# Kernel tuning notes

Hardware: AMD Instinct MI355X
Metric: run time of the kernel (lower is better)

Reference implementation:

```python
import jax, jax.numpy as jnp
import numpy as np

NUM_HEADS = 16
KEY_DEPTH = 1024


def setup_inputs() -> dict:
    key = jax.random.key(0)
    ks = jax.random.split(key, 7)
    B, L, D = 2, 2048, 1024
    scale = 1.0 / np.sqrt(D)
    return {
        "query_antecedent": jax.random.normal(ks[0], (B, L, D), jnp.float32),
        "memory_antecedent": jax.random.normal(ks[1], (B, L, D), jnp.float32),
        "bias": jax.random.normal(ks[2], (1, 1, L, L), jnp.float32),
        "Wq": jax.random.normal(ks[3], (D, KEY_DEPTH), jnp.float32) * scale,
        "Wk": jax.random.normal(ks[4], (D, KEY_DEPTH), jnp.float32) * scale,
        "Wv": jax.random.normal(ks[5], (D, KEY_DEPTH), jnp.float32) * scale,
        "Wo": jax.random.normal(ks[6], (KEY_DEPTH, D), jnp.float32) * scale,
    }


def _split_heads(x, h):
    # [B, L, D] -> [B, H, L, D/H]
    b, l, d = x.shape
    return x.reshape(b, l, h, d // h).transpose(0, 2, 1, 3)


def reference(query_antecedent, memory_antecedent, bias, Wq, Wk, Wv, Wo):
    h = NUM_HEADS
    d_head = KEY_DEPTH // h
    q = _split_heads(query_antecedent @ Wq, h) * (d_head ** -0.5)
    k = _split_heads(memory_antecedent @ Wk, h)
    v = _split_heads(memory_antecedent @ Wv, h)
    # [B, H, Lq, Lk]
    logits = jnp.einsum("bhqd,bhkd->bhqk", q, k) + bias
    weights = jax.nn.softmax(logits, axis=-1)
    x = jnp.einsum("bhqk,bhkd->bhqd", weights, v)
    # combine heads: [B, H, L, d] -> [B, L, H*d]
    b, _, l, d = x.shape
    x = x.transpose(0, 2, 1, 3).reshape(b, l, h * d)
    return x @ Wo
```

## Files before the change

### kernel.cpp

```cpp
#include <hip/hip_runtime.h>
#include <hip/hip_bf16.h>


typedef __attribute__((ext_vector_type(8))) short short8;
typedef __attribute__((ext_vector_type(4))) short short4v;
typedef __attribute__((ext_vector_type(4))) float float4v;

#define BATCH 2
#define LSEQ 2048
#define DMODEL 1024
#define NHEADS 16
#define DHEAD 64
#define MROWS 4096
#define QKVLD 3072

__global__ __launch_bounds__(256)
void convert_kernel(const float* __restrict__ qa, const float* __restrict__ ma,
                    __hip_bfloat16* __restrict__ qo, __hip_bfloat16* __restrict__ mo)
{
    const size_t i = ((size_t)blockIdx.x * 256 + threadIdx.x) * 8;
    const float* src = blockIdx.y ? ma : qa;
    __hip_bfloat16* dst = blockIdx.y ? mo : qo;
    float4 v0 = *reinterpret_cast<const float4*>(src + i);
    float4 v1 = *reinterpret_cast<const float4*>(src + i + 4);
    union { __hip_bfloat16 h[8]; int4 v; } pk;
    pk.h[0] = (__hip_bfloat16)v0.x; pk.h[1] = (__hip_bfloat16)v0.y;
    pk.h[2] = (__hip_bfloat16)v0.z; pk.h[3] = (__hip_bfloat16)v0.w;
    pk.h[4] = (__hip_bfloat16)v1.x; pk.h[5] = (__hip_bfloat16)v1.y;
    pk.h[6] = (__hip_bfloat16)v1.z; pk.h[7] = (__hip_bfloat16)v1.w;
    *reinterpret_cast<int4*>(dst + i) = pk.v;
}

__global__ __launch_bounds__(256)
void transpose_w_kernel(const float* __restrict__ W0, const float* __restrict__ W1,
                        const float* __restrict__ W2, const float* __restrict__ W3,
                        __hip_bfloat16* __restrict__ T0, __hip_bfloat16* __restrict__ T1,
                        __hip_bfloat16* __restrict__ T2, __hip_bfloat16* __restrict__ T3)
{
    __shared__ __hip_bfloat16 T[64][68];

    const float* W; __hip_bfloat16* D;
    if      (blockIdx.z == 0) { W = W0; D = T0; }
    else if (blockIdx.z == 1) { W = W1; D = T1; }
    else if (blockIdx.z == 2) { W = W2; D = T2; }
    else                      { W = W3; D = T3; }

    const int t  = threadIdx.x;
    const int n0 = blockIdx.x * 64;
    const int k0 = blockIdx.y * 64;

#pragma unroll
    for (int p = 0; p < 4; ++p) {
        const int r = p * 16 + (t >> 4);
        const int c = (t & 15) * 4;
        float4 v = *reinterpret_cast<const float4*>(&W[(size_t)(k0 + r) * DMODEL + n0 + c]);
        union { __hip_bfloat16 h[4]; ushort4 v; } pk;
        pk.h[0] = (__hip_bfloat16)v.x; pk.h[1] = (__hip_bfloat16)v.y;
        pk.h[2] = (__hip_bfloat16)v.z; pk.h[3] = (__hip_bfloat16)v.w;
        *reinterpret_cast<ushort4*>(&T[r][c]) = pk.v;
    }
    __syncthreads();
#pragma unroll
    for (int p = 0; p < 2; ++p) {
        const int n  = p * 32 + (t & 31);
        const int kc = (t >> 5) * 8;
        union { __hip_bfloat16 h[8]; int4 v; } pk;
#pragma unroll
        for (int j = 0; j < 8; ++j) pk.h[j] = T[kc + j][n];
        *reinterpret_cast<int4*>(&D[(size_t)(n0 + n) * DMODEL + k0 + kc]) = pk.v;
    }
}

#define GBK 64

__global__ __launch_bounds__(256, 2)
void gemm_bt_kernel(const __hip_bfloat16* __restrict__ A0,
                    const __hip_bfloat16* __restrict__ A1, int nsplit,
                    float alpha0, float alpha1,
                    const __hip_bfloat16* __restrict__ Bt,
                    float* __restrict__ Cf, __hip_bfloat16* __restrict__ Cb,
                    int K, int ldc, int nbx)
{
    __shared__ __hip_bfloat16 As[128][GBK];
    __shared__ __hip_bfloat16 Bs[128][GBK];

    const int t    = threadIdx.x;
    const int w    = t >> 6;
    const int lane = t & 63;
    const int l15  = lane & 15;
    const int lq   = lane >> 4;
    const int wm   = (w >> 1) * 64;
    const int wn   = (w & 1) * 64;

    const int nwg  = gridDim.x;
    const int c    = blockIdx.x & 7;
    const int q    = blockIdx.x >> 3;
    const int mper = (nwg >> 3) / nbx;
    const int m0   = (c * mper + q / nbx) * 128;
    const int n0   = (q % nbx) * 128;

    const __hip_bfloat16* A = (n0 < nsplit) ? A0 : A1;
    const float alpha = (n0 < nsplit) ? alpha0 : alpha1;

    const int lrow = lane >> 3;
    const int lch  = (lane & 7) ^ lrow;

    float4v acc[4][4];
#pragma unroll
    for (int mi = 0; mi < 4; ++mi)
#pragma unroll
        for (int ni = 0; ni < 4; ++ni) acc[mi][ni] = (float4v){0.f, 0.f, 0.f, 0.f};

    for (int k0 = 0; k0 < K; k0 += GBK) {
        __syncthreads();
#pragma unroll
        for (int i = 0; i < 4; ++i) {
            const int rb = (w * 4 + i) * 8;
            const int r  = rb + lrow;
            __builtin_amdgcn_global_load_lds(
                (const __attribute__((address_space(1))) void*)
                    (A + (size_t)(m0 + r) * K + k0 + lch * 8),
                (__attribute__((address_space(3))) void*)&As[rb][0], 16, 0, 0);
            __builtin_amdgcn_global_load_lds(
                (const __attribute__((address_space(1))) void*)
                    (Bt + (size_t)(n0 + r) * K + k0 + lch * 8),
                (__attribute__((address_space(3))) void*)&Bs[rb][0], 16, 0, 0);
        }
        asm volatile("s_waitcnt vmcnt(0)" ::: "memory");
        __syncthreads();

#pragma unroll
        for (int kh = 0; kh < 2; ++kh) {
            short8 af[4], bf[4];
#pragma unroll
            for (int mi = 0; mi < 4; ++mi) {
                const int r = wm + mi * 16 + l15;
                af[mi] = *reinterpret_cast<const short8*>(
                    &As[r][(((kh << 2) | lq) ^ (r & 7)) << 3]);
            }
#pragma unroll
            for (int ni = 0; ni < 4; ++ni) {
                const int r = wn + ni * 16 + l15;
                bf[ni] = *reinterpret_cast<const short8*>(
                    &Bs[r][(((kh << 2) | lq) ^ (r & 7)) << 3]);
            }
#pragma unroll
            for (int mi = 0; mi < 4; ++mi)
#pragma unroll
                for (int ni = 0; ni < 4; ++ni)
                    acc[mi][ni] = __builtin_amdgcn_mfma_f32_16x16x32_bf16(
                        af[mi], bf[ni], acc[mi][ni], 0, 0, 0);
        }
    }

#pragma unroll
    for (int mi = 0; mi < 4; ++mi)
#pragma unroll
        for (int ni = 0; ni < 4; ++ni)
#pragma unroll
            for (int r = 0; r < 4; ++r) {
                const int row = m0 + wm + mi * 16 + lq * 4 + r;
                const int col = n0 + wn + ni * 16 + l15;
                const float v = acc[mi][ni][r] * alpha;
                if (Cf) Cf[(size_t)row * ldc + col] = v;
                else    Cb[(size_t)row * ldc + col] = (__hip_bfloat16)v;
            }
}

#define KSTR 68
#define PSTR 132

__global__ __launch_bounds__(512, 4)
void attn_mfma_kernel(const __hip_bfloat16* __restrict__ QKV,
                      const float* __restrict__ bias,
                      __hip_bfloat16* __restrict__ X)
{
    __shared__ __hip_bfloat16 Ks[128][KSTR];
    __shared__ __hip_bfloat16 Vt[64][PSTR];

    const int t   = threadIdx.x;
    const int w   = t >> 6;
    const int l15 = t & 15;
    const int lq  = (t & 63) >> 4;

    const int bid = blockIdx.x;
    const int r8  = bid & 7;
    const int j   = bid >> 3;
    const int bh  = r8 + 8 * (j >> 4);
    const int q0  = (j & 15) * 128;
    const int b   = bh >> 4;
    const int h   = bh & 15;

    const __hip_bfloat16* Kb = QKV + (size_t)b * LSEQ * QKVLD + 1024 + h * DHEAD;
    const __hip_bfloat16* Vb = Kb + 1024;

    short8 aq[2];
    {
        const __hip_bfloat16* qrow = QKV +
            (size_t)(b * LSEQ + q0 + w * 16 + l15) * QKVLD + h * DHEAD + lq * 8;
        aq[0] = *reinterpret_cast<const short8*>(qrow);
        aq[1] = *reinterpret_cast<const short8*>(qrow + 32);
    }

    const float* bp = bias + (size_t)(q0 + w * 16 + l15) * LSEQ + lq * 4;

    float lsum = 0.f;
    float4v o_acc[4];
#pragma unroll
    for (int n = 0; n < 4; ++n) o_acc[n] = (float4v){0.f, 0.f, 0.f, 0.f};

    const int skey = t >> 2;
    const int sdh  = (t & 3) * 16;
    const int a    = t & 3;
    const int cblk = ((skey >> 5) << 2) | ((skey >> 2) & 3);
    const int vcol = (((cblk ^ (a << 2)) << 3)) | ((((skey >> 4) & 1) << 2)) | (skey & 3);

    int4 pk0, pk1, pv0, pv1;
    {
        const __hip_bfloat16* ks = Kb + (size_t)skey * QKVLD + sdh;
        pk0 = *reinterpret_cast<const int4*>(ks);
        pk1 = *reinterpret_cast<const int4*>(ks + 8);
        const __hip_bfloat16* vs = Vb + (size_t)skey * QKVLD + sdh;
        pv0 = *reinterpret_cast<const int4*>(vs);
        pv1 = *reinterpret_cast<const int4*>(vs + 8);
    }

    for (int kt = 0; kt < LSEQ / 128; ++kt) {
        const int k0 = kt * 128;
        __syncthreads();
        *reinterpret_cast<int4*>(&Ks[skey][sdh])     = pk0;
        *reinterpret_cast<int4*>(&Ks[skey][sdh + 8]) = pk1;
        {
            const __hip_bfloat16* vp0 = reinterpret_cast<const __hip_bfloat16*>(&pv0);
            const __hip_bfloat16* vp1 = reinterpret_cast<const __hip_bfloat16*>(&pv1);
#pragma unroll
            for (int jj = 0; jj < 8; ++jj) Vt[sdh + jj][vcol]     = vp0[jj];
#pragma unroll
            for (int jj = 0; jj < 8; ++jj) Vt[sdh + 8 + jj][vcol] = vp1[jj];
        }
        {
            const int knext = (kt + 1 < LSEQ / 128) ? k0 + 128 : k0;
            const __hip_bfloat16* ks = Kb + (size_t)(knext + skey) * QKVLD + sdh;
            pk0 = *reinterpret_cast<const int4*>(ks);
            pk1 = *reinterpret_cast<const int4*>(ks + 8);
            const __hip_bfloat16* vs = Vb + (size_t)(knext + skey) * QKVLD + sdh;
            pv0 = *reinterpret_cast<const int4*>(vs);
            pv1 = *reinterpret_cast<const int4*>(vs + 8);
        }
        __syncthreads();

#pragma unroll
        for (int m = 0; m < 4; ++m) {
            short8 bkA0 = *reinterpret_cast<const short8*>(&Ks[(2*m)    *16 + l15][lq * 8]);
            short8 bkA1 = *reinterpret_cast<const short8*>(&Ks[(2*m)    *16 + l15][32 + lq * 8]);
            short8 bkB0 = *reinterpret_cast<const short8*>(&Ks[(2*m + 1)*16 + l15][lq * 8]);
            short8 bkB1 = *reinterpret_cast<const short8*>(&Ks[(2*m + 1)*16 + l15][32 + lq * 8]);
            float4v bvA = *reinterpret_cast<const float4v*>(bp + k0 + 32 * m);
            float4v bvB = *reinterpret_cast<const float4v*>(bp + k0 + 32 * m + 16);

            float4v sA = (float4v){0.f, 0.f, 0.f, 0.f};
            float4v sB = (float4v){0.f, 0.f, 0.f, 0.f};
            __builtin_amdgcn_s_setprio(1);
            sA = __builtin_amdgcn_mfma_f32_16x16x32_bf16(bkA0, aq[0], sA, 0, 0, 0);
            sA = __builtin_amdgcn_mfma_f32_16x16x32_bf16(bkA1, aq[1], sA, 0, 0, 0);
            sB = __builtin_amdgcn_mfma_f32_16x16x32_bf16(bkB0, aq[0], sB, 0, 0, 0);
            sB = __builtin_amdgcn_mfma_f32_16x16x32_bf16(bkB1, aq[1], sB, 0, 0, 0);
            __builtin_amdgcn_s_setprio(0);

            union { __hip_bfloat16 hh[8]; short8 v; } pp;
#pragma unroll
            for (int r = 0; r < 4; ++r) {
                const float e = __expf(sA[r] + bvA[r]);
                lsum += e;
                pp.hh[r] = (__hip_bfloat16)e;
            }
#pragma unroll
            for (int r = 0; r < 4; ++r) {
                const float e = __expf(sB[r] + bvB[r]);
                lsum += e;
                pp.hh[4 + r] = (__hip_bfloat16)e;
            }
            const short8 pf = pp.v;

            short8 vt[4];
#pragma unroll
            for (int n = 0; n < 4; ++n)
                vt[n] = *reinterpret_cast<const short8*>(
                    &Vt[n * 16 + l15][((m * 4 + lq) ^ (n << 2)) << 3]);

            __builtin_amdgcn_s_setprio(1);
#pragma unroll
            for (int n = 0; n < 4; ++n)
                o_acc[n] = __builtin_amdgcn_mfma_f32_16x16x32_bf16(
                    vt[n], pf, o_acc[n], 0, 0, 0);
            __builtin_amdgcn_s_setprio(0);
        }
    }

    lsum += __shfl_xor(lsum, 16);
    lsum += __shfl_xor(lsum, 32);
    const float inv = 1.f / lsum;
    {
        const int row = q0 + w * 16 + l15;
        __hip_bfloat16* dst = X + (size_t)(b * LSEQ + row) * DMODEL + h * DHEAD + lq * 4;
#pragma unroll
        for (int n = 0; n < 4; ++n) {
            union { __hip_bfloat16 hh[4]; short4v v; } o;
#pragma unroll
            for (int r = 0; r < 4; ++r) o.hh[r] = (__hip_bfloat16)(o_acc[n][r] * inv);
            *reinterpret_cast<short4v*>(dst + n * 16) = o.v;
        }
    }
}

extern "C" void kernel_launch(void* const* d_in, const int* in_sizes, int n_in,
                              void* d_out, int out_size, void* d_ws, size_t ws_size,
                              hipStream_t stream)
{
    const float* qa   = (const float*)d_in[0];
    const float* ma   = (const float*)d_in[1];
    const float* bias = (const float*)d_in[2];
    const float* Wq   = (const float*)d_in[3];
    const float* Wk   = (const float*)d_in[4];
    const float* Wv   = (const float*)d_in[5];
    const float* Wo   = (const float*)d_in[6];
    float* out = (float*)d_out;

    char* wsb = (char*)d_ws;
    __hip_bfloat16* qa16 = (__hip_bfloat16*)(wsb);
    __hip_bfloat16* ma16 = (__hip_bfloat16*)(wsb + (8u << 20));
    __hip_bfloat16* Wt   = (__hip_bfloat16*)(wsb + (16u << 20));
    __hip_bfloat16* Wot  = (__hip_bfloat16*)(wsb + (22u << 20));
    __hip_bfloat16* QKVw = (__hip_bfloat16*)(wsb + (24u << 20));
    __hip_bfloat16* Xw   = qa16;

    convert_kernel<<<dim3(MROWS * DMODEL / (256 * 8), 2), 256, 0, stream>>>(
        qa, ma, qa16, ma16);

    transpose_w_kernel<<<dim3(16, 16, 4), 256, 0, stream>>>(
        Wq, Wk, Wv, Wo,
        Wt, Wt + (size_t)DMODEL * DMODEL, Wt + 2 * (size_t)DMODEL * DMODEL, Wot);

    gemm_bt_kernel<<<dim3(768), 256, 0, stream>>>(
        qa16, ma16, DMODEL, 0.125f, 1.0f, Wt, nullptr, QKVw, DMODEL, QKVLD, 24);

    attn_mfma_kernel<<<dim3(512), 512, 0, stream>>>(QKVw, bias, Xw);

    gemm_bt_kernel<<<dim3(256), 256, 0, stream>>>(
        Xw, Xw, DMODEL + 1, 1.0f, 1.0f, Wot, out, nullptr, DMODEL, DMODEL, 8);
}
```

Before: 240.8 us.

## Process two query tiles per attention warp and shrink the output GEMM tile

The attention kernel now has each wave handle 32 query rows instead of 16, so every K/V tile staged in LDS is reused by two MFMA groups. This halves the grid to 256 blocks and lowers the occupancy hint to 2. Separately, the output projection GEMM is templated to use 64-row M tiles, doubling its grid to 512 blocks to fill more CUs. The trade-offs are higher register pressure and fewer blocks in attention, plus less reuse per block in the output GEMM.

New measurement: 249.4 us. 1.04x slower.

```diff
diff --git a/kernel.cpp b/kernel.cpp
--- a/kernel.cpp
+++ b/kernel.cpp
@@ -73,6 +73,7 @@
 
 #define GBK 64
 
+template<int BMT>
 __global__ __launch_bounds__(256, 2)
 void gemm_bt_kernel(const __hip_bfloat16* __restrict__ A0,
                     const __hip_bfloat16* __restrict__ A1, int nsplit,
@@ -81,7 +82,7 @@
                     float* __restrict__ Cf, __hip_bfloat16* __restrict__ Cb,
                     int K, int ldc, int nbx)
 {
-    __shared__ __hip_bfloat16 As[128][GBK];
+    __shared__ __hip_bfloat16 As[BMT][GBK];
     __shared__ __hip_bfloat16 Bs[128][GBK];
 
     const int t    = threadIdx.x;
@@ -89,14 +90,15 @@
     const int lane = t & 63;
     const int l15  = lane & 15;
     const int lq   = lane >> 4;
-    const int wm   = (w >> 1) * 64;
+    const int wm   = (w >> 1) * (BMT / 2);
     const int wn   = (w & 1) * 64;
+    const int MI   = BMT / 32;
 
     const int nwg  = gridDim.x;
     const int c    = blockIdx.x & 7;
     const int q    = blockIdx.x >> 3;
     const int mper = (nwg >> 3) / nbx;
-    const int m0   = (c * mper + q / nbx) * 128;
+    const int m0   = (c * mper + q / nbx) * BMT;
     const int n0   = (q % nbx) * 128;
 
     const __hip_bfloat16* A = (n0 < nsplit) ? A0 : A1;
@@ -105,24 +107,29 @@
     const int lrow = lane >> 3;
     const int lch  = (lane & 7) ^ lrow;
 
-    float4v acc[4][4];
-#pragma unroll
-    for (int mi = 0; mi < 4; ++mi)
+    float4v acc[BMT / 32][4];
+#pragma unroll
+    for (int mi = 0; mi < MI; ++mi)
 #pragma unroll
         for (int ni = 0; ni < 4; ++ni) acc[mi][ni] = (float4v){0.f, 0.f, 0.f, 0.f};
 
     for (int k0 = 0; k0 < K; k0 += GBK) {
         __syncthreads();
+#pragma unroll
+        for (int i = 0; i < BMT / 32; ++i) {
+            const int rb = (w * (BMT / 32) + i) * 8;
+            const int r  = rb + lrow;
+            __builtin_amdgcn_global_load_lds(
+                (const __attribute__((address_space(1))) void*)
+                    (A + (size_t)(m0 + r) * K + k0 + lch * 8),
+                (__attribute__((address_space(3))) void*)&As[rb][0], 16, 0, 0);
+        }
 #pragma unroll
         for (int i = 0; i < 4; ++i) {
             const int rb = (w * 4 + i) * 8;
             const int r  = rb + lrow;
             __builtin_amdgcn_global_load_lds(
                 (const __attribute__((address_space(1))) void*)
-                    (A + (size_t)(m0 + r) * K + k0 + lch * 8),
-                (__attribute__((address_space(3))) void*)&As[rb][0], 16, 0, 0);
-            __builtin_amdgcn_global_load_lds(
-                (const __attribute__((address_space(1))) void*)
                     (Bt + (size_t)(n0 + r) * K + k0 + lch * 8),
                 (__attribute__((address_space(3))) void*)&Bs[rb][0], 16, 0, 0);
         }
@@ -131,9 +138,9 @@
 
 #pragma unroll
         for (int kh = 0; kh < 2; ++kh) {
-            short8 af[4], bf[4];
-#pragma unroll
-            for (int mi = 0; mi < 4; ++mi) {
+            short8 af[BMT / 32], bf[4];
+#pragma unroll
+            for (int mi = 0; mi < MI; ++mi) {
                 const int r = wm + mi * 16 + l15;
                 af[mi] = *reinterpret_cast<const short8*>(
                     &As[r][(((kh << 2) | lq) ^ (r & 7)) << 3]);
@@ -145,7 +152,7 @@
                     &Bs[r][(((kh << 2) | lq) ^ (r & 7)) << 3]);
             }
 #pragma unroll
-            for (int mi = 0; mi < 4; ++mi)
+            for (int mi = 0; mi < MI; ++mi)
 #pragma unroll
                 for (int ni = 0; ni < 4; ++ni)
                     acc[mi][ni] = __builtin_amdgcn_mfma_f32_16x16x32_bf16(
@@ -154,7 +161,7 @@
     }
 
 #pragma unroll
-    for (int mi = 0; mi < 4; ++mi)
+    for (int mi = 0; mi < MI; ++mi)
 #pragma unroll
         for (int ni = 0; ni < 4; ++ni)
 #pragma unroll
@@ -170,7 +177,7 @@
 #define KSTR 68
 #define PSTR 132
 
-__global__ __launch_bounds__(512, 4)
+__global__ __launch_bounds__(512, 2)
 void attn_mfma_kernel(const __hip_bfloat16* __restrict__ QKV,
                       const float* __restrict__ bias,
                       __hip_bfloat16* __restrict__ X)
@@ -186,28 +193,32 @@
     const int bid = blockIdx.x;
     const int r8  = bid & 7;
     const int j   = bid >> 3;
-    const int bh  = r8 + 8 * (j >> 4);
-    const int q0  = (j & 15) * 128;
+    const int bh  = r8 + 8 * (j >> 3);
+    const int q0  = (j & 7) * 256;
     const int b   = bh >> 4;
     const int h   = bh & 15;
 
     const __hip_bfloat16* Kb = QKV + (size_t)b * LSEQ * QKVLD + 1024 + h * DHEAD;
     const __hip_bfloat16* Vb = Kb + 1024;
 
-    short8 aq[2];
-    {
+    short8 aq[2][2];
+#pragma unroll
+    for (int g = 0; g < 2; ++g) {
         const __hip_bfloat16* qrow = QKV +
-            (size_t)(b * LSEQ + q0 + w * 16 + l15) * QKVLD + h * DHEAD + lq * 8;
-        aq[0] = *reinterpret_cast<const short8*>(qrow);
-        aq[1] = *reinterpret_cast<const short8*>(qrow + 32);
-    }
-
-    const float* bp = bias + (size_t)(q0 + w * 16 + l15) * LSEQ + lq * 4;
-
-    float lsum = 0.f;
-    float4v o_acc[4];
-#pragma unroll
-    for (int n = 0; n < 4; ++n) o_acc[n] = (float4v){0.f, 0.f, 0.f, 0.f};
+            (size_t)(b * LSEQ + q0 + w * 32 + g * 16 + l15) * QKVLD + h * DHEAD + lq * 8;
+        aq[g][0] = *reinterpret_cast<const short8*>(qrow);
+        aq[g][1] = *reinterpret_cast<const short8*>(qrow + 32);
+    }
+
+    const float* bp0 = bias + (size_t)(q0 + w * 32 + l15) * LSEQ + lq * 4;
+    const float* bp1 = bp0 + (size_t)16 * LSEQ;
+
+    float lsum[2] = {0.f, 0.f};
+    float4v o_acc[2][4];
+#pragma unroll
+    for (int g = 0; g < 2; ++g)
+#pragma unroll
+        for (int n = 0; n < 4; ++n) o_acc[g][n] = (float4v){0.f, 0.f, 0.f, 0.f};
 
     const int skey = t >> 2;
     const int sdh  = (t & 3) * 16;
@@ -255,32 +266,44 @@
             short8 bkA1 = *reinterpret_cast<const short8*>(&Ks[(2*m)    *16 + l15][32 + lq * 8]);
             short8 bkB0 = *reinterpret_cast<const short8*>(&Ks[(2*m + 1)*16 + l15][lq * 8]);
             short8 bkB1 = *reinterpret_cast<const short8*>(&Ks[(2*m + 1)*16 + l15][32 + lq * 8]);
-            float4v bvA = *reinterpret_cast<const float4v*>(bp + k0 + 32 * m);
-            float4v bvB = *reinterpret_cast<const float4v*>(bp + k0 + 32 * m + 16);
-
-            float4v sA = (float4v){0.f, 0.f, 0.f, 0.f};
-            float4v sB = (float4v){0.f, 0.f, 0.f, 0.f};
+
+            float4v sA[2], sB[2];
+#pragma unroll
+            for (int g = 0; g < 2; ++g) {
+                sA[g] = (float4v){0.f, 0.f, 0.f, 0.f};
+                sB[g] = (float4v){0.f, 0.f, 0.f, 0.f};
+            }
             __builtin_amdgcn_s_setprio(1);
-            sA = __builtin_amdgcn_mfma_f32_16x16x32_bf16(bkA0, aq[0], sA, 0, 0, 0);
-            sA = __builtin_amdgcn_mfma_f32_16x16x32_bf16(bkA1, aq[1], sA, 0, 0, 0);
-            sB = __builtin_amdgcn_mfma_f32_16x16x32_bf16(bkB0, aq[0], sB, 0, 0, 0);
-            sB = __builtin_amdgcn_mfma_f32_16x16x32_bf16(bkB1, aq[1], sB, 0, 0, 0);
+#pragma unroll
+            for (int g = 0; g < 2; ++g) {
+                sA[g] = __builtin_amdgcn_mfma_f32_16x16x32_bf16(bkA0, aq[g][0], sA[g], 0, 0, 0);
+                sA[g] = __builtin_amdgcn_mfma_f32_16x16x32_bf16(bkA1, aq[g][1], sA[g], 0, 0, 0);
+                sB[g] = __builtin_amdgcn_mfma_f32_16x16x32_bf16(bkB0, aq[g][0], sB[g], 0, 0, 0);
+                sB[g] = __builtin_amdgcn_mfma_f32_16x16x32_bf16(bkB1, aq[g][1], sB[g], 0, 0, 0);
+            }
             __builtin_amdgcn_s_setprio(0);
 
-            union { __hip_bfloat16 hh[8]; short8 v; } pp;
-#pragma unroll
-            for (int r = 0; r < 4; ++r) {
-                const float e = __expf(sA[r] + bvA[r]);
-                lsum += e;
-                pp.hh[r] = (__hip_bfloat16)e;
-            }
-#pragma unroll
-            for (int r = 0; r < 4; ++r) {
-                const float e = __expf(sB[r] + bvB[r]);
-                lsum += e;
-                pp.hh[4 + r] = (__hip_bfloat16)e;
-            }
-            const short8 pf = pp.v;
+            short8 pf[2];
+#pragma unroll
+            for (int g = 0; g < 2; ++g) {
+                const float* bp = g ? bp1 : bp0;
+                float4v bvA = *reinterpret_cast<const float4v*>(bp + k0 + 32 * m);
+                float4v bvB = *reinterpret_cast<const float4v*>(bp + k0 + 32 * m + 16);
+                union { __hip_bfloat16 hh[8]; short8 v; } pp;
+#pragma unroll
+                for (int r = 0; r < 4; ++r) {
+                    const float e = __expf(sA[g][r] + bvA[r]);
+                    lsum[g] += e;
+                    pp.hh[r] = (__hip_bfloat16)e;
+                }
+#pragma unroll
+                for (int r = 0; r < 4; ++r) {
+                    const float e = __expf(sB[g][r] + bvB[r]);
+                    lsum[g] += e;
+                    pp.hh[4 + r] = (__hip_bfloat16)e;
+                }
+                pf[g] = pp.v;
+            }
 
             short8 vt[4];
 #pragma unroll
@@ -290,24 +313,27 @@
 
             __builtin_amdgcn_s_setprio(1);
 #pragma unroll
-            for (int n = 0; n < 4; ++n)
-                o_acc[n] = __builtin_amdgcn_mfma_f32_16x16x32_bf16(
-                    vt[n], pf, o_acc[n], 0, 0, 0);
+            for (int g = 0; g < 2; ++g)
+#pragma unroll
+                for (int n = 0; n < 4; ++n)
+                    o_acc[g][n] = __builtin_amdgcn_mfma_f32_16x16x32_bf16(
+                        vt[n], pf[g], o_acc[g][n], 0, 0, 0);
             __builtin_amdgcn_s_setprio(0);
         }
     }
 
-    lsum += __shfl_xor(lsum, 16);
-    lsum += __shfl_xor(lsum, 32);
-    const float inv = 1.f / lsum;
-    {
-        const int row = q0 + w * 16 + l15;
+#pragma unroll
+    for (int g = 0; g < 2; ++g) {
+        lsum[g] += __shfl_xor(lsum[g], 16);
+        lsum[g] += __shfl_xor(lsum[g], 32);
+        const float inv = 1.f / lsum[g];
+        const int row = q0 + w * 32 + g * 16 + l15;
         __hip_bfloat16* dst = X + (size_t)(b * LSEQ + row) * DMODEL + h * DHEAD + lq * 4;
 #pragma unroll
         for (int n = 0; n < 4; ++n) {
             union { __hip_bfloat16 hh[4]; short4v v; } o;
 #pragma unroll
-            for (int r = 0; r < 4; ++r) o.hh[r] = (__hip_bfloat16)(o_acc[n][r] * inv);
+            for (int r = 0; r < 4; ++r) o.hh[r] = (__hip_bfloat16)(o_acc[g][n][r] * inv);
             *reinterpret_cast<short4v*>(dst + n * 16) = o.v;
         }
     }
@@ -341,11 +367,11 @@
         Wq, Wk, Wv, Wo,
         Wt, Wt + (size_t)DMODEL * DMODEL, Wt + 2 * (size_t)DMODEL * DMODEL, Wot);
 
-    gemm_bt_kernel<<<dim3(768), 256, 0, stream>>>(
+    gemm_bt_kernel<128><<<dim3(768), 256, 0, stream>>>(
         qa16, ma16, DMODEL, 0.125f, 1.0f, Wt, nullptr, QKVw, DMODEL, QKVLD, 24);
 
-    attn_mfma_kernel<<<dim3(512), 512, 0, stream>>>(QKVw, bias, Xw);
-
-    gemm_bt_kernel<<<dim3(256), 256, 0, stream>>>(
+    attn_mfma_kernel<<<dim3(256), 512, 0, stream>>>(QKVw, bias, Xw);
+
+    gemm_bt_kernel<64><<<dim3(512), 256, 0, stream>>>(
         Xw, Xw, DMODEL + 1, 1.0f, 1.0f, Wot, out, nullptr, DMODEL, DMODEL, 8);
 }
```

## Double-buffer attention K/V tiles and use 64-row tiles for output GEMM

Applied to the files above, without the earlier changes.

The attention kernel now keeps two LDS buffers for K and V^T. The next tile is written into the spare buffer while the current one is consumed, which drops one of the two barriers per iteration and lets LDS stores overlap MFMA work. The GEMM kernel is templated on the M tile size, and the output projection runs with 64-row tiles on 512 blocks instead of 256, to fill more CUs. The cost is twice the LDS in attention, which may cut occupancy, and less B-tile reuse per block in the output GEMM.

Result: faster. 235.2 us (-2.3%).

```diff
diff --git a/kernel.cpp b/kernel.cpp
--- a/kernel.cpp
+++ b/kernel.cpp
@@ -73,6 +73,7 @@
 
 #define GBK 64
 
+template<int BMT>
 __global__ __launch_bounds__(256, 2)
 void gemm_bt_kernel(const __hip_bfloat16* __restrict__ A0,
                     const __hip_bfloat16* __restrict__ A1, int nsplit,
@@ -81,7 +82,7 @@
                     float* __restrict__ Cf, __hip_bfloat16* __restrict__ Cb,
                     int K, int ldc, int nbx)
 {
-    __shared__ __hip_bfloat16 As[128][GBK];
+    __shared__ __hip_bfloat16 As[BMT][GBK];
     __shared__ __hip_bfloat16 Bs[128][GBK];
 
     const int t    = threadIdx.x;
@@ -89,14 +90,15 @@
     const int lane = t & 63;
     const int l15  = lane & 15;
     const int lq   = lane >> 4;
-    const int wm   = (w >> 1) * 64;
+    const int wm   = (w >> 1) * (BMT / 2);
     const int wn   = (w & 1) * 64;
+    const int MI   = BMT / 32;
 
     const int nwg  = gridDim.x;
     const int c    = blockIdx.x & 7;
     const int q    = blockIdx.x >> 3;
     const int mper = (nwg >> 3) / nbx;
-    const int m0   = (c * mper + q / nbx) * 128;
+    const int m0   = (c * mper + q / nbx) * BMT;
     const int n0   = (q % nbx) * 128;
 
     const __hip_bfloat16* A = (n0 < nsplit) ? A0 : A1;
@@ -105,24 +107,29 @@
     const int lrow = lane >> 3;
     const int lch  = (lane & 7) ^ lrow;
 
-    float4v acc[4][4];
-#pragma unroll
-    for (int mi = 0; mi < 4; ++mi)
+    float4v acc[BMT / 32][4];
+#pragma unroll
+    for (int mi = 0; mi < MI; ++mi)
 #pragma unroll
         for (int ni = 0; ni < 4; ++ni) acc[mi][ni] = (float4v){0.f, 0.f, 0.f, 0.f};
 
     for (int k0 = 0; k0 < K; k0 += GBK) {
         __syncthreads();
+#pragma unroll
+        for (int i = 0; i < BMT / 32; ++i) {
+            const int rb = (w * (BMT / 32) + i) * 8;
+            const int r  = rb + lrow;
+            __builtin_amdgcn_global_load_lds(
+                (const __attribute__((address_space(1))) void*)
+                    (A + (size_t)(m0 + r) * K + k0 + lch * 8),
+                (__attribute__((address_space(3))) void*)&As[rb][0], 16, 0, 0);
+        }
 #pragma unroll
         for (int i = 0; i < 4; ++i) {
             const int rb = (w * 4 + i) * 8;
             const int r  = rb + lrow;
             __builtin_amdgcn_global_load_lds(
                 (const __attribute__((address_space(1))) void*)
-                    (A + (size_t)(m0 + r) * K + k0 + lch * 8),
-                (__attribute__((address_space(3))) void*)&As[rb][0], 16, 0, 0);
-            __builtin_amdgcn_global_load_lds(
-                (const __attribute__((address_space(1))) void*)
                     (Bt + (size_t)(n0 + r) * K + k0 + lch * 8),
                 (__attribute__((address_space(3))) void*)&Bs[rb][0], 16, 0, 0);
         }
@@ -131,9 +138,9 @@
 
 #pragma unroll
         for (int kh = 0; kh < 2; ++kh) {
-            short8 af[4], bf[4];
-#pragma unroll
-            for (int mi = 0; mi < 4; ++mi) {
+            short8 af[BMT / 32], bf[4];
+#pragma unroll
+            for (int mi = 0; mi < MI; ++mi) {
                 const int r = wm + mi * 16 + l15;
                 af[mi] = *reinterpret_cast<const short8*>(
                     &As[r][(((kh << 2) | lq) ^ (r & 7)) << 3]);
@@ -145,7 +152,7 @@
                     &Bs[r][(((kh << 2) | lq) ^ (r & 7)) << 3]);
             }
 #pragma unroll
-            for (int mi = 0; mi < 4; ++mi)
+            for (int mi = 0; mi < MI; ++mi)
 #pragma unroll
                 for (int ni = 0; ni < 4; ++ni)
                     acc[mi][ni] = __builtin_amdgcn_mfma_f32_16x16x32_bf16(
@@ -154,7 +161,7 @@
     }
 
 #pragma unroll
-    for (int mi = 0; mi < 4; ++mi)
+    for (int mi = 0; mi < MI; ++mi)
 #pragma unroll
         for (int ni = 0; ni < 4; ++ni)
 #pragma unroll
@@ -169,14 +176,15 @@
 
 #define KSTR 68
 #define PSTR 132
+#define NT (LSEQ / 128)
 
 __global__ __launch_bounds__(512, 4)
 void attn_mfma_kernel(const __hip_bfloat16* __restrict__ QKV,
                       const float* __restrict__ bias,
                       __hip_bfloat16* __restrict__ X)
 {
-    __shared__ __hip_bfloat16 Ks[128][KSTR];
-    __shared__ __hip_bfloat16 Vt[64][PSTR];
+    __shared__ __hip_bfloat16 Ks[2][128][KSTR];
+    __shared__ __hip_bfloat16 Vt[2][64][PSTR];
 
     const int t   = threadIdx.x;
     const int w   = t >> 6;
@@ -224,37 +232,56 @@
         pv0 = *reinterpret_cast<const int4*>(vs);
         pv1 = *reinterpret_cast<const int4*>(vs + 8);
     }
-
-    for (int kt = 0; kt < LSEQ / 128; ++kt) {
-        const int k0 = kt * 128;
-        __syncthreads();
-        *reinterpret_cast<int4*>(&Ks[skey][sdh])     = pk0;
-        *reinterpret_cast<int4*>(&Ks[skey][sdh + 8]) = pk1;
-        {
+    *reinterpret_cast<int4*>(&Ks[0][skey][sdh])     = pk0;
+    *reinterpret_cast<int4*>(&Ks[0][skey][sdh + 8]) = pk1;
+    {
+        const __hip_bfloat16* vp0 = reinterpret_cast<const __hip_bfloat16*>(&pv0);
+        const __hip_bfloat16* vp1 = reinterpret_cast<const __hip_bfloat16*>(&pv1);
+#pragma unroll
+        for (int jj = 0; jj < 8; ++jj) Vt[0][sdh + jj][vcol]     = vp0[jj];
+#pragma unroll
+        for (int jj = 0; jj < 8; ++jj) Vt[0][sdh + 8 + jj][vcol] = vp1[jj];
+    }
+    {
+        const __hip_bfloat16* ks = Kb + (size_t)(128 + skey) * QKVLD + sdh;
+        pk0 = *reinterpret_cast<const int4*>(ks);
+        pk1 = *reinterpret_cast<const int4*>(ks + 8);
+        const __hip_bfloat16* vs = Vb + (size_t)(128 + skey) * QKVLD + sdh;
+        pv0 = *reinterpret_cast<const int4*>(vs);
+        pv1 = *reinterpret_cast<const int4*>(vs + 8);
+    }
+    __syncthreads();
+
+    for (int kt = 0; kt < NT; ++kt) {
+        const int cur = kt & 1;
+        const int k0  = kt * 128;
+
+        if (kt < NT - 1) {
+            *reinterpret_cast<int4*>(&Ks[cur ^ 1][skey][sdh])     = pk0;
+            *reinterpret_cast<int4*>(&Ks[cur ^ 1][skey][sdh + 8]) = pk1;
             const __hip_bfloat16* vp0 = reinterpret_cast<const __hip_bfloat16*>(&pv0);
             const __hip_bfloat16* vp1 = reinterpret_cast<const __hip_bfloat16*>(&pv1);
 #pragma unroll
-            for (int jj = 0; jj < 8; ++jj) Vt[sdh + jj][vcol]     = vp0[jj];
-#pragma unroll
-            for (int jj = 0; jj < 8; ++jj) Vt[sdh + 8 + jj][vcol] = vp1[jj];
-        }
-        {
-            const int knext = (kt + 1 < LSEQ / 128) ? k0 + 128 : k0;
-            const __hip_bfloat16* ks = Kb + (size_t)(knext + skey) * QKVLD + sdh;
-            pk0 = *reinterpret_cast<const int4*>(ks);
-            pk1 = *reinterpret_cast<const int4*>(ks + 8);
-            const __hip_bfloat16* vs = Vb + (size_t)(knext + skey) * QKVLD + sdh;
-            pv0 = *reinterpret_cast<const int4*>(vs);
-            pv1 = *reinterpret_cast<const int4*>(vs + 8);
-        }
-        __syncthreads();
+            for (int jj = 0; jj < 8; ++jj) Vt[cur ^ 1][sdh + jj][vcol]     = vp0[jj];
+#pragma unroll
+            for (int jj = 0; jj < 8; ++jj) Vt[cur ^ 1][sdh + 8 + jj][vcol] = vp1[jj];
+            if (kt < NT - 2) {
+                const int knext = k0 + 256;
+                const __hip_bfloat16* ks = Kb + (size_t)(knext + skey) * QKVLD + sdh;
+                pk0 = *reinterpret_cast<const int4*>(ks);
+                pk1 = *reinterpret_cast<const int4*>(ks + 8);
+                const __hip_bfloat16* vs = Vb + (size_t)(knext + skey) * QKVLD + sdh;
+                pv0 = *reinterpret_cast<const int4*>(vs);
+                pv1 = *reinterpret_cast<const int4*>(vs + 8);
+            }
+        }
 
 #pragma unroll
         for (int m = 0; m < 4; ++m) {
-            short8 bkA0 = *reinterpret_cast<const short8*>(&Ks[(2*m)    *16 + l15][lq * 8]);
-            short8 bkA1 = *reinterpret_cast<const short8*>(&Ks[(2*m)    *16 + l15][32 + lq * 8]);
-            short8 bkB0 = *reinterpret_cast<const short8*>(&Ks[(2*m + 1)*16 + l15][lq * 8]);
-            short8 bkB1 = *reinterpret_cast<const short8*>(&Ks[(2*m + 1)*16 + l15][32 + lq * 8]);
+            short8 bkA0 = *reinterpret_cast<const short8*>(&Ks[cur][(2*m)    *16 + l15][lq * 8]);
+            short8 bkA1 = *reinterpret_cast<const short8*>(&Ks[cur][(2*m)    *16 + l15][32 + lq * 8]);
+            short8 bkB0 = *reinterpret_cast<const short8*>(&Ks[cur][(2*m + 1)*16 + l15][lq * 8]);
+            short8 bkB1 = *reinterpret_cast<const short8*>(&Ks[cur][(2*m + 1)*16 + l15][32 + lq * 8]);
             float4v bvA = *reinterpret_cast<const float4v*>(bp + k0 + 32 * m);
             float4v bvB = *reinterpret_cast<const float4v*>(bp + k0 + 32 * m + 16);
 
@@ -269,16 +296,16 @@
 
             union { __hip_bfloat16 hh[8]; short8 v; } pp;
 #pragma unroll
-            for (int r = 0; r < 4; ++r) {
-                const float e = __expf(sA[r] + bvA[r]);
-                lsum += e;
-                pp.hh[r] = (__hip_bfloat16)e;
-            }
-#pragma unroll
-            for (int r = 0; r < 4; ++r) {
-                const float e = __expf(sB[r] + bvB[r]);
-                lsum += e;
-                pp.hh[4 + r] = (__hip_bfloat16)e;
+            for (int e = 0; e < 4; ++e) {
+                const float ev = __expf(sA[e] + bvA[e]);
+                lsum += ev;
+                pp.hh[e] = (__hip_bfloat16)ev;
+            }
+#pragma unroll
+            for (int e = 0; e < 4; ++e) {
+                const float ev = __expf(sB[e] + bvB[e]);
+                lsum += ev;
+                pp.hh[4 + e] = (__hip_bfloat16)ev;
             }
             const short8 pf = pp.v;
 
@@ -286,7 +313,7 @@
 #pragma unroll
             for (int n = 0; n < 4; ++n)
                 vt[n] = *reinterpret_cast<const short8*>(
-                    &Vt[n * 16 + l15][((m * 4 + lq) ^ (n << 2)) << 3]);
+                    &Vt[cur][n * 16 + l15][((m * 4 + lq) ^ (n << 2)) << 3]);
 
             __builtin_amdgcn_s_setprio(1);
 #pragma unroll
@@ -295,6 +322,7 @@
                     vt[n], pf, o_acc[n], 0, 0, 0);
             __builtin_amdgcn_s_setprio(0);
         }
+        __syncthreads();
     }
 
     lsum += __shfl_xor(lsum, 16);
@@ -307,7 +335,7 @@
         for (int n = 0; n < 4; ++n) {
             union { __hip_bfloat16 hh[4]; short4v v; } o;
 #pragma unroll
-            for (int r = 0; r < 4; ++r) o.hh[r] = (__hip_bfloat16)(o_acc[n][r] * inv);
+            for (int e = 0; e < 4; ++e) o.hh[e] = (__hip_bfloat16)(o_acc[n][e] * inv);
             *reinterpret_cast<short4v*>(dst + n * 16) = o.v;
         }
     }
@@ -341,11 +369,11 @@
         Wq, Wk, Wv, Wo,
         Wt, Wt + (size_t)DMODEL * DMODEL, Wt + 2 * (size_t)DMODEL * DMODEL, Wot);
 
-    gemm_bt_kernel<<<dim3(768), 256, 0, stream>>>(
+    gemm_bt_kernel<128><<<dim3(768), 256, 0, stream>>>(
         qa16, ma16, DMODEL, 0.125f, 1.0f, Wt, nullptr, QKVw, DMODEL, QKVLD, 24);
 
     attn_mfma_kernel<<<dim3(512), 512, 0, stream>>>(QKVw, bias, Xw);
 
-    gemm_bt_kernel<<<dim3(256), 256, 0, stream>>>(
+    gemm_bt_kernel<64><<<dim3(512), 256, 0, stream>>>(
         Xw, Xw, DMODEL + 1, 1.0f, 1.0f, Wot, out, nullptr, DMODEL, DMODEL, 8);
 }
```
